# Kernel tuning notes

Hardware: AMD Instinct MI355X
Metric: run time of the kernel (lower is better)

## Reference

```python
import jax, jax.numpy as jnp
import numpy as np

HEADS = 8
HEAD_DIM = 64
WINDOW = 65  # odd


def setup_inputs() -> dict:
    key = jax.random.key(0)
    k1, k2, k3 = jax.random.split(key, 3)
    B, S, D_MODEL = 2, 2048, HEADS * HEAD_DIM
    x = jax.random.normal(k1, (B, S, D_MODEL), dtype=jnp.float32)
    W_qkv = jax.random.normal(k2, (D_MODEL, 3 * HEADS * HEAD_DIM), dtype=jnp.float32) * (1.0 / np.sqrt(D_MODEL))
    W_out = jax.random.normal(k3, (HEADS * HEAD_DIM, D_MODEL), dtype=jnp.float32) * (1.0 / np.sqrt(HEADS * HEAD_DIM))
    b_out = jnp.zeros((D_MODEL,), dtype=jnp.float32)
    return {"x": x, "W_qkv": W_qkv, "W_out": W_out, "b_out": b_out}


def reference(x, W_qkv, W_out, b_out):
    B, S, _ = x.shape
    H, D, W = HEADS, HEAD_DIM, WINDOW
    pad = W // 2

    qkv = x @ W_qkv                              # [B,S,3*H*D]
    qkv = qkv.reshape(B, S, H, 3 * D)
    q, k, v = jnp.split(qkv, 3, axis=-1)          # each [B,S,H,D]

    # zero-pad along sequence (matches tf.pad; padded keys get score 0, NOT -inf)
    k_pad = jnp.pad(k, ((0, 0), (pad, pad), (0, 0), (0, 0)))
    v_pad = jnp.pad(v, ((0, 0), (pad, pad), (0, 0), (0, 0)))

    # sliding windows via gather: [S, W] indices into padded seq (= tf.signal.frame)
    idx = jnp.arange(S)[:, None] + jnp.arange(W)[None, :]
    k_win = k_pad[:, idx]                         # [B,S,W,H,D]
    v_win = v_pad[:, idx]                         # [B,S,W,H,D]

    scale = 1.0 / jnp.sqrt(jnp.asarray(D, dtype=x.dtype))
    scores = jnp.einsum('bshd,bswhd->bhsw', q, k_win) * scale  # [B,H,S,W]
    weights = jax.nn.softmax(scores, axis=-1)
    attn = jnp.einsum('bhsw,bswhd->bshd', weights, v_win)       # [B,S,H,D]
    attn = attn.reshape(B, S, H * D)
    return attn @ W_out + b_out
```

## Files before the change

kernel.cpp:

```cpp
#include <hip/hip_runtime.h>
#include <hip/hip_bf16.h>
#include <stdint.h>

typedef short short8 __attribute__((ext_vector_type(8)));
typedef float f32x4 __attribute__((ext_vector_type(4)));
typedef unsigned short ushort4_t __attribute__((ext_vector_type(4)));
typedef unsigned short ushort8_t __attribute__((ext_vector_type(8)));

#define S_LEN 2048
#define NQKV 1536
#define DMODEL 512

__device__ inline unsigned short f2bf(float f) {
  unsigned int u = __float_as_uint(f);
  unsigned int r = (u + 0x7FFFu + ((u >> 16) & 1u)) >> 16;
  return (unsigned short)r;
}

__device__ __forceinline__ void gll16(const unsigned short* g, unsigned short* l) {
  __builtin_amdgcn_global_load_lds(
      (const __attribute__((address_space(1))) unsigned int*)g,
      (__attribute__((address_space(3))) unsigned int*)l, 16, 0, 0);
}

__global__ __launch_bounds__(256) void k_prep(const float* __restrict__ x,
                                              unsigned short* __restrict__ xb,
                                              const float* __restrict__ w1,
                                              unsigned short* __restrict__ o1,
                                              const float* __restrict__ w2,
                                              unsigned short* __restrict__ o2) {
  __shared__ float T[32][33];
  int bid = blockIdx.x;
  int t = threadIdx.x;
  if (bid < 1024) {
    int i = (bid * 256 + t) * 8;
    float4 a = *(const float4*)(x + i);
    float4 b = *(const float4*)(x + i + 4);
    ushort8_t o;
    o[0] = f2bf(a.x); o[1] = f2bf(a.y); o[2] = f2bf(a.z); o[3] = f2bf(a.w);
    o[4] = f2bf(b.x); o[5] = f2bf(b.y); o[6] = f2bf(b.z); o[7] = f2bf(b.w);
    *(ushort8_t*)(xb + i) = o;
    return;
  }
  bid -= 1024;
  int bx = bid & 63, byy = bid >> 6;
  const float* w; unsigned short* o; int cols;
  if (bx < 48) { w = w1; o = o1; cols = 1536; }
  else         { w = w2; o = o2; cols = 512; bx -= 48; }
  int r0 = byy * 32, c0 = bx * 32;
  int tr = t / 32, tc = t % 32;
#pragma unroll
  for (int i = 0; i < 4; i++) {
    int r = tr + i * 8;
    T[r][tc] = w[(size_t)(r0 + r) * cols + c0 + tc];
  }
  __syncthreads();
#pragma unroll
  for (int i = 0; i < 4; i++) {
    int rr = tr + i * 8;
    o[(size_t)(c0 + rr) * 512 + r0 + tc] = f2bf(T[tc][rr]);
  }
}

template <int BM, int MODE>
__global__ __launch_bounds__(256) void k_gemm(const unsigned short* __restrict__ A,
                                              const unsigned short* __restrict__ Bt,
                                              void* __restrict__ Cout,
                                              const float* __restrict__ bias,
                                              unsigned short* __restrict__ vt,
                                              int M, int N, int K) {
  constexpr int MR = BM / 32;
  constexpr int CA = BM / 64;
  constexpr int STAGE_SH = 2 * BM * 32 + 2 * 128 * 32;
  constexpr int SMEM_SH = (MODE == 1 && 128 * 128 > STAGE_SH) ? 128 * 128 : STAGE_SH;
  __shared__ __align__(16) unsigned short smem[SMEM_SH];
  const int ASZ = BM * 32, BOFF = 2 * BM * 32, BSZ = 128 * 32;

  const int t = threadIdx.x, lane = t & 63, wid = t >> 6;
  const int m0 = blockIdx.y * BM, n0 = blockIdx.x * 128;
  const int wm = (wid >> 1) * (BM / 2), wn = (wid & 1) * 64;
  const int lr = lane & 15, kr = (lane >> 4) * 8, lg = lane >> 4;
  const unsigned short* Ab = A + (size_t)m0 * K;
  const unsigned short* Bb = Bt + (size_t)n0 * K;
  f32x4 acc[MR][4] = {};

  const int NT = K / 32;
  auto stage = [&](int buf, int kt) {
#pragma unroll
    for (int c = 0; c < CA; c++) {
      int f = t + 256 * c;
      gll16(Ab + (size_t)(f >> 2) * K + kt + (f & 3) * 8, &smem[buf * ASZ + f * 8]);
    }
#pragma unroll
    for (int c = 0; c < 2; c++) {
      int f = t + 256 * c;
      gll16(Bb + (size_t)(f >> 2) * K + kt + (f & 3) * 8, &smem[BOFF + buf * BSZ + f * 8]);
    }
  };

  stage(0, 0);
  int buf = 0;
  for (int it = 0; it < NT; ++it) {
    __syncthreads();
    if (it + 1 < NT) stage(buf ^ 1, (it + 1) * 32);
    const unsigned short* Ap = &smem[buf * ASZ];
    const unsigned short* Bp = &smem[BOFF + buf * BSZ];
    short8 af[MR], bfv[4];
#pragma unroll
    for (int i = 0; i < MR; i++)
      af[i] = *(const short8*)&Ap[(wm + i * 16 + lr) * 32 + kr];
#pragma unroll
    for (int i = 0; i < 4; i++)
      bfv[i] = *(const short8*)&Bp[(wn + i * 16 + lr) * 32 + kr];
#pragma unroll
    for (int mi = 0; mi < MR; mi++)
#pragma unroll
      for (int ni = 0; ni < 4; ni++)
        acc[mi][ni] = __builtin_amdgcn_mfma_f32_16x16x32_bf16(af[mi], bfv[ni], acc[mi][ni], 0, 0, 0);
    buf ^= 1;
  }

  if (MODE == 0) {
#pragma unroll
    for (int mi = 0; mi < MR; mi++) {
#pragma unroll
      for (int ni = 0; ni < 4; ni++) {
        int col = n0 + wn + ni * 16 + lr;
        float bv = bias[col];
#pragma unroll
        for (int j = 0; j < 4; j++) {
          int row = m0 + wm + mi * 16 + lg * 4 + j;
          ((float*)Cout)[(size_t)row * N + col] = acc[mi][ni][j] + bv;
        }
      }
    }
  } else {
    __syncthreads();
#pragma unroll
    for (int mi = 0; mi < MR; mi++)
#pragma unroll
      for (int ni = 0; ni < 4; ni++)
#pragma unroll
        for (int j = 0; j < 4; j++) {
          int row = wm + mi * 16 + lg * 4 + j;
          int col = wn + ni * 16 + lr;
          smem[row * 128 + (col ^ (((row >> 3) & 7) << 3))] = f2bf(acc[mi][ni][j]);
        }
    __syncthreads();

    unsigned short* qkvout = (unsigned short*)Cout;
    const int b_ = m0 >> 11;
    const int posb = m0 & 2047;
#pragma unroll
    for (int hf = 0; hf < 2; hf++) {
      int c_abs = n0 + hf * 64;
      int g = c_abs % 192;
      if (g < 128) {
#pragma unroll
        for (int i = 0; i < 4; i++) {
          int s = t + 256 * i;
          int row = s >> 3, ch = s & 7;
          int src = row * 128 + ((hf * 64 + ch * 8) ^ (((row >> 3) & 7) << 3));
          ushort8_t v = *(const ushort8_t*)&smem[src];
          *(ushort8_t*)&qkvout[(size_t)(m0 + row) * NQKV + c_abs + ch * 8] = v;
        }
      } else {
        int h = c_abs / 192, d0 = g - 128;
#pragma unroll
        for (int i = 0; i < 4; i++) {
          int s = t + 256 * i;
          int dl = s >> 4, pc = s & 15;
          ushort8_t v;
#pragma unroll
          for (int j = 0; j < 8; j++) {
            int row = pc * 8 + j;
            v[j] = smem[row * 128 + ((hf * 64 + dl) ^ (((row >> 3) & 7) << 3))];
          }
          *(ushort8_t*)&vt[((size_t)((b_ * 8 + h) * 64 + d0 + dl)) * 2048 + posb + pc * 8] = v;
        }
      }
    }
  }
}

__global__ __launch_bounds__(256) void k_attn(const unsigned short* __restrict__ qkv,
                                              const unsigned short* __restrict__ vT,
                                              unsigned short* __restrict__ attn) {
  const int t = threadIdx.x, lane = t & 63, w = t >> 6;
  const int blk = blockIdx.x;
  const int sbi = blk & 31, h = (blk >> 5) & 7, b = blk >> 8;
  const int sb = sbi * 64;
  const unsigned short* base = qkv + (size_t)b * S_LEN * NQKV;
  const int lr = lane & 15, lg = lane >> 4;
  const int s0 = sb + w * 16;

  short8 qb[2];
#pragma unroll
  for (int ks = 0; ks < 2; ks++)
    qb[ks] = *(const short8*)(base + (size_t)(s0 + lr) * NQKV + h * 192 + ks * 32 + lg * 8);

  f32x4 sc[5] = {};
#pragma unroll
  for (int ct = 0; ct < 5; ct++) {
    int p = s0 - 32 + ct * 16 + lr;
    bool inb = (p >= 0 && p < S_LEN);
#pragma unroll
    for (int ks = 0; ks < 2; ks++) {
      short8 ka = {};
      if (inb)
        ka = *(const short8*)(base + (size_t)p * NQKV + h * 192 + 64 + ks * 32 + lg * 8);
      sc[ct] = __builtin_amdgcn_mfma_f32_16x16x32_bf16(ka, qb[ks], sc[ct], 0, 0, 0);
    }
  }

  float mx = -1e30f;
#pragma unroll
  for (int ct = 0; ct < 5; ct++)
#pragma unroll
    for (int j = 0; j < 4; j++) {
      int c2 = ct * 16 + lg * 4 + j;
      sc[ct][j] = (c2 >= lr && c2 <= lr + 64) ? sc[ct][j] * 0.125f : -1e30f;
      mx = fmaxf(mx, sc[ct][j]);
    }
  mx = fmaxf(mx, __shfl_xor(mx, 16, 64));
  mx = fmaxf(mx, __shfl_xor(mx, 32, 64));

  float pn[5][4];
  float sum = 0.0f;
#pragma unroll
  for (int ct = 0; ct < 5; ct++)
#pragma unroll
    for (int j = 0; j < 4; j++) {
      pn[ct][j] = __expf(sc[ct][j] - mx);
      sum += pn[ct][j];
    }
  sum += __shfl_xor(sum, 16, 64);
  sum += __shfl_xor(sum, 32, 64);
  float inv = 1.0f / sum;

  unsigned int w01[5], w23[5];
#pragma unroll
  for (int ct = 0; ct < 5; ct++) {
    float v[4];
#pragma unroll
    for (int j = 0; j < 4; j++) {
      int p = s0 - 32 + ct * 16 + lg * 4 + j;
      float xv = pn[ct][j] * inv;
      v[j] = (p >= 0 && p < S_LEN) ? xv : 0.0f;
    }
    w01[ct] = (unsigned int)f2bf(v[0]) | ((unsigned int)f2bf(v[1]) << 16);
    w23[ct] = (unsigned int)f2bf(v[2]) | ((unsigned int)f2bf(v[3]) << 16);
  }

  const unsigned short* vbase = vT + (size_t)((b * 8 + h) * 64) * 2048;
  f32x4 oa[4] = {};
  const int h2 = lg & 1, tl = lg >> 1;
  const int sA = 32 * h2 + lr, sB = sA + 16;
#pragma unroll
  for (int ks = 0; ks < 3; ks++) {
    const int T0 = 2 * ks;
    const int T1 = (2 * ks + 1 < 5) ? (2 * ks + 1) : 4;
    unsigned int a0 = __shfl((int)w01[T0], sA, 64), a1 = __shfl((int)w23[T0], sA, 64);
    unsigned int a2 = __shfl((int)w01[T0], sB, 64), a3 = __shfl((int)w23[T0], sB, 64);
    unsigned int b0 = __shfl((int)w01[T1], sA, 64), b1 = __shfl((int)w23[T1], sA, 64);
    unsigned int b2 = __shfl((int)w01[T1], sB, 64), b3 = __shfl((int)w23[T1], sB, 64);
    union { unsigned int u[4]; short8 v; } pb;
    pb.u[0] = tl ? b0 : a0;
    pb.u[1] = tl ? b1 : a1;
    pb.u[2] = tl ? b2 : a2;
    pb.u[3] = tl ? b3 : a3;
    if (ks == 2 && tl) { pb.u[0] = 0; pb.u[1] = 0; pb.u[2] = 0; pb.u[3] = 0; }
    int poff = s0 - 32 + ks * 32 + lg * 8;
#pragma unroll
    for (int nt = 0; nt < 4; nt++) {
      short8 va = *(const short8*)(vbase + (size_t)(nt * 16 + lr) * 2048 + poff);
      oa[nt] = __builtin_amdgcn_mfma_f32_16x16x32_bf16(va, pb.v, oa[nt], 0, 0, 0);
    }
  }

#pragma unroll
  for (int nt = 0; nt < 4; nt++) {
    ushort4_t o;
#pragma unroll
    for (int j = 0; j < 4; j++) o[j] = f2bf(oa[nt][j]);
    *(ushort4_t*)(attn + ((size_t)b * S_LEN + s0 + lr) * DMODEL + h * 64 + nt * 16 + lg * 4) = o;
  }
}

extern "C" void kernel_launch(void* const* d_in, const int* in_sizes, int n_in,
                              void* d_out, int out_size, void* d_ws, size_t ws_size,
                              hipStream_t stream) {
  const float* x    = (const float*)d_in[0];
  const float* Wqkv = (const float*)d_in[1];
  const float* Wout = (const float*)d_in[2];
  const float* bout = (const float*)d_in[3];
  char* ws = (char*)d_ws;
  unsigned short* xb    = (unsigned short*)(ws + 0);
  unsigned short* wqkvt = (unsigned short*)(ws + 4194304);
  unsigned short* woutt = (unsigned short*)(ws + 5767168);
  unsigned short* qkv   = (unsigned short*)(ws + 6291456);
  unsigned short* attn  = (unsigned short*)(ws + 18874368);
  unsigned short* vT    = (unsigned short*)(ws + 23068672);

  hipLaunchKernelGGL(k_prep, dim3(2048), dim3(256), 0, stream,
                     x, xb, Wqkv, wqkvt, Wout, woutt);
  hipLaunchKernelGGL((k_gemm<128, 1>), dim3(12, 32), dim3(256), 0, stream,
                     xb, wqkvt, (void*)qkv, (const float*)nullptr, vT, 4096, 1536, 512);
  hipLaunchKernelGGL(k_attn, dim3(512), dim3(256), 0, stream, qkv, vT, attn);
  hipLaunchKernelGGL((k_gemm<64, 0>), dim3(4, 64), dim3(256), 0, stream,
                     attn, woutt, d_out, bout, (unsigned short*)nullptr, 4096, 512, 512);
}
```

Baseline: 44.31 us.

## Store Q/K/V in per-head zero-padded layouts and stage attention tiles in LDS

The QKV GEMM epilogue now writes Q as contiguous per-head rows, and writes K and V (transposed) into per-head buffers padded by 32 zero rows on each side. The padding is cleared by extra blocks in the prep kernel. The attention kernel loads its K, V and Q tiles into swizzled LDS with async global-to-LDS loads instead of strided global reads, which removes the per-element bounds checks and masking. The output GEMM epilogue now goes through LDS so it can write coalesced float4 stores with the bias added. The cost is more LDS use in the attention kernel and extra zero-fill work in the prep kernel.

```diff
diff --git a/kernel.cpp b/kernel.cpp
--- a/kernel.cpp
+++ b/kernel.cpp
@@ -28,7 +28,9 @@
                                               const float* __restrict__ w1,
                                               unsigned short* __restrict__ o1,
                                               const float* __restrict__ w2,
-                                              unsigned short* __restrict__ o2) {
+                                              unsigned short* __restrict__ o2,
+                                              unsigned short* __restrict__ Kp,
+                                              unsigned short* __restrict__ Vp) {
   __shared__ float T[32][33];
   int bid = blockIdx.x;
   int t = threadIdx.x;
@@ -42,6 +44,29 @@
     *(ushort8_t*)(xb + i) = o;
     return;
   }
+  if (bid >= 2048) {
+    int p = bid - 2048;
+    ushort8_t z = {};
+    if (p < 16) {
+      unsigned short* dst = Kp + (size_t)p * 2112 * 64;
+#pragma unroll
+      for (int i = 0; i < 2; i++) {
+        int s = t + 256 * i;
+        int row = s >> 3, c = s & 7;
+        int r2 = row < 32 ? row : row - 32 + 2080;
+        *(ushort8_t*)&dst[r2 * 64 + c * 8] = z;
+      }
+    } else {
+      unsigned short* dst = Vp + (size_t)(p - 16) * 64 * 2112;
+#pragma unroll
+      for (int i = 0; i < 2; i++) {
+        int s = t + 256 * i;
+        int d = s >> 3, side = (s >> 2) & 1, c = s & 3;
+        *(ushort8_t*)&dst[(size_t)d * 2112 + side * 2080 + c * 8] = z;
+      }
+    }
+    return;
+  }
   bid -= 1024;
   int bx = bid & 63, byy = bid >> 6;
   const float* w; unsigned short* o; int cols;
@@ -67,12 +92,15 @@
                                               const unsigned short* __restrict__ Bt,
                                               void* __restrict__ Cout,
                                               const float* __restrict__ bias,
-                                              unsigned short* __restrict__ vt,
+                                              unsigned short* __restrict__ qs,
+                                              unsigned short* __restrict__ kp,
+                                              unsigned short* __restrict__ vp,
                                               int M, int N, int K) {
   constexpr int MR = BM / 32;
   constexpr int CA = BM / 64;
   constexpr int STAGE_SH = 2 * BM * 32 + 2 * 128 * 32;
-  constexpr int SMEM_SH = (MODE == 1 && 128 * 128 > STAGE_SH) ? 128 * 128 : STAGE_SH;
+  constexpr int BOUNCE_SH = 16384;
+  constexpr int SMEM_SH = STAGE_SH > BOUNCE_SH ? STAGE_SH : BOUNCE_SH;
   __shared__ __align__(16) unsigned short smem[SMEM_SH];
   const int ASZ = BM * 32, BOFF = 2 * BM * 32, BSZ = 128 * 32;
 
@@ -121,18 +149,24 @@
   }
 
   if (MODE == 0) {
-#pragma unroll
-    for (int mi = 0; mi < MR; mi++) {
-#pragma unroll
-      for (int ni = 0; ni < 4; ni++) {
-        int col = n0 + wn + ni * 16 + lr;
-        float bv = bias[col];
-#pragma unroll
-        for (int j = 0; j < 4; j++) {
-          int row = m0 + wm + mi * 16 + lg * 4 + j;
-          ((float*)Cout)[(size_t)row * N + col] = acc[mi][ni][j] + bv;
-        }
-      }
+    __syncthreads();
+    float* ft = (float*)smem;
+#pragma unroll
+    for (int mi = 0; mi < MR; mi++)
+#pragma unroll
+      for (int ni = 0; ni < 4; ni++)
+#pragma unroll
+        for (int j = 0; j < 4; j++)
+          ft[(wm + mi * 16 + lg * 4 + j) * 128 + wn + ni * 16 + lr] = acc[mi][ni][j];
+    __syncthreads();
+#pragma unroll
+    for (int i = 0; i < BM / 8; i++) {
+      int s = t + 256 * i;
+      int row = s >> 5, ch = s & 31;
+      float4 v = *(const float4*)&ft[row * 128 + ch * 4];
+      float4 bv = *(const float4*)&bias[n0 + ch * 4];
+      v.x += bv.x; v.y += bv.y; v.z += bv.z; v.w += bv.w;
+      *(float4*)&((float*)Cout)[(size_t)(m0 + row) * N + n0 + ch * 4] = v;
     }
   } else {
     __syncthreads();
@@ -148,24 +182,25 @@
         }
     __syncthreads();
 
-    unsigned short* qkvout = (unsigned short*)Cout;
     const int b_ = m0 >> 11;
     const int posb = m0 & 2047;
 #pragma unroll
     for (int hf = 0; hf < 2; hf++) {
       int c_abs = n0 + hf * 64;
-      int g = c_abs % 192;
-      if (g < 128) {
+      int h = c_abs / 192, seg = (c_abs % 192) >> 6;
+      if (seg < 2) {
+        unsigned short* dst = (seg == 0)
+            ? qs + ((size_t)(b_ * 8 + h) * 2048 + posb) * 64
+            : kp + ((size_t)(b_ * 8 + h) * 2112 + 32 + posb) * 64;
 #pragma unroll
         for (int i = 0; i < 4; i++) {
           int s = t + 256 * i;
           int row = s >> 3, ch = s & 7;
           int src = row * 128 + ((hf * 64 + ch * 8) ^ (((row >> 3) & 7) << 3));
-          ushort8_t v = *(const ushort8_t*)&smem[src];
-          *(ushort8_t*)&qkvout[(size_t)(m0 + row) * NQKV + c_abs + ch * 8] = v;
+          *(ushort8_t*)&dst[s * 8] = *(const ushort8_t*)&smem[src];
         }
       } else {
-        int h = c_abs / 192, d0 = g - 128;
+        unsigned short* dst = vp + (size_t)(b_ * 8 + h) * 64 * 2112;
 #pragma unroll
         for (int i = 0; i < 4; i++) {
           int s = t + 256 * i;
@@ -176,39 +211,66 @@
             int row = pc * 8 + j;
             v[j] = smem[row * 128 + ((hf * 64 + dl) ^ (((row >> 3) & 7) << 3))];
           }
-          *(ushort8_t*)&vt[((size_t)((b_ * 8 + h) * 64 + d0 + dl)) * 2048 + posb + pc * 8] = v;
+          *(ushort8_t*)&dst[(size_t)dl * 2112 + 32 + posb + pc * 8] = v;
         }
       }
     }
   }
 }
 
-__global__ __launch_bounds__(256) void k_attn(const unsigned short* __restrict__ qkv,
-                                              const unsigned short* __restrict__ vT,
-                                              unsigned short* __restrict__ attn) {
+__global__ __launch_bounds__(256) void k_attn(const unsigned short* __restrict__ Qs,
+                                              const unsigned short* __restrict__ Kp,
+                                              const unsigned short* __restrict__ Vp,
+                                              unsigned short* __restrict__ attnb) {
+  __shared__ __align__(16) unsigned short Kt[128 * 64];
+  __shared__ __align__(16) unsigned short Vt[64 * 192];
+  __shared__ __align__(16) unsigned short Qt[64 * 64];
   const int t = threadIdx.x, lane = t & 63, w = t >> 6;
   const int blk = blockIdx.x;
   const int sbi = blk & 31, h = (blk >> 5) & 7, b = blk >> 8;
   const int sb = sbi * 64;
-  const unsigned short* base = qkv + (size_t)b * S_LEN * NQKV;
+  const int bh = b * 8 + h;
   const int lr = lane & 15, lg = lane >> 4;
-  const int s0 = sb + w * 16;
+
+  {
+    const unsigned short* src = Kp + ((size_t)bh * 2112 + sb) * 64;
+#pragma unroll
+    for (int i = 0; i < 4; i++) {
+      int s = t + 256 * i, row = s >> 3, c = s & 7;
+      gll16(src + row * 64 + (c ^ (row & 7)) * 8, &Kt[s * 8]);
+    }
+  }
+  {
+    const unsigned short* src = Vp + (size_t)bh * 64 * 2112 + sb;
+#pragma unroll
+    for (int i = 0; i < 6; i++) {
+      int s = t + 256 * i, d = s / 24, c = s - d * 24;
+      gll16(src + (size_t)d * 2112 + (c ^ (d & 7)) * 8, &Vt[s * 8]);
+    }
+  }
+  {
+    const unsigned short* src = Qs + ((size_t)bh * 2048 + sb) * 64;
+#pragma unroll
+    for (int i = 0; i < 2; i++) {
+      int s = t + 256 * i, row = s >> 3, c = s & 7;
+      gll16(src + row * 64 + (c ^ (row & 7)) * 8, &Qt[s * 8]);
+    }
+  }
+  __syncthreads();
+
+  const int sw = (lr & 7) << 3;
 
   short8 qb[2];
 #pragma unroll
   for (int ks = 0; ks < 2; ks++)
-    qb[ks] = *(const short8*)(base + (size_t)(s0 + lr) * NQKV + h * 192 + ks * 32 + lg * 8);
+    qb[ks] = *(const short8*)&Qt[(w * 16 + lr) * 64 + ((ks * 32 + lg * 8) ^ sw)];
 
   f32x4 sc[5] = {};
 #pragma unroll
   for (int ct = 0; ct < 5; ct++) {
-    int p = s0 - 32 + ct * 16 + lr;
-    bool inb = (p >= 0 && p < S_LEN);
 #pragma unroll
     for (int ks = 0; ks < 2; ks++) {
-      short8 ka = {};
-      if (inb)
-        ka = *(const short8*)(base + (size_t)p * NQKV + h * 192 + 64 + ks * 32 + lg * 8);
+      short8 ka = *(const short8*)&Kt[(w * 16 + ct * 16 + lr) * 64 + ((ks * 32 + lg * 8) ^ sw)];
       sc[ct] = __builtin_amdgcn_mfma_f32_16x16x32_bf16(ka, qb[ks], sc[ct], 0, 0, 0);
     }
   }
@@ -241,18 +303,10 @@
   unsigned int w01[5], w23[5];
 #pragma unroll
   for (int ct = 0; ct < 5; ct++) {
-    float v[4];
-#pragma unroll
-    for (int j = 0; j < 4; j++) {
-      int p = s0 - 32 + ct * 16 + lg * 4 + j;
-      float xv = pn[ct][j] * inv;
-      v[j] = (p >= 0 && p < S_LEN) ? xv : 0.0f;
-    }
-    w01[ct] = (unsigned int)f2bf(v[0]) | ((unsigned int)f2bf(v[1]) << 16);
-    w23[ct] = (unsigned int)f2bf(v[2]) | ((unsigned int)f2bf(v[3]) << 16);
-  }
-
-  const unsigned short* vbase = vT + (size_t)((b * 8 + h) * 64) * 2048;
+    w01[ct] = (unsigned int)f2bf(pn[ct][0] * inv) | ((unsigned int)f2bf(pn[ct][1] * inv) << 16);
+    w23[ct] = (unsigned int)f2bf(pn[ct][2] * inv) | ((unsigned int)f2bf(pn[ct][3] * inv) << 16);
+  }
+
   f32x4 oa[4] = {};
   const int h2 = lg & 1, tl = lg >> 1;
   const int sA = 32 * h2 + lr, sB = sA + 16;
@@ -270,20 +324,21 @@
     pb.u[2] = tl ? b2 : a2;
     pb.u[3] = tl ? b3 : a3;
     if (ks == 2 && tl) { pb.u[0] = 0; pb.u[1] = 0; pb.u[2] = 0; pb.u[3] = 0; }
-    int poff = s0 - 32 + ks * 32 + lg * 8;
+    int pofl = w * 16 + ks * 32 + lg * 8;
 #pragma unroll
     for (int nt = 0; nt < 4; nt++) {
-      short8 va = *(const short8*)(vbase + (size_t)(nt * 16 + lr) * 2048 + poff);
+      short8 va = *(const short8*)&Vt[(nt * 16 + lr) * 192 + (pofl ^ sw)];
       oa[nt] = __builtin_amdgcn_mfma_f32_16x16x32_bf16(va, pb.v, oa[nt], 0, 0, 0);
     }
   }
 
+  const int s0 = sb + w * 16;
 #pragma unroll
   for (int nt = 0; nt < 4; nt++) {
     ushort4_t o;
 #pragma unroll
     for (int j = 0; j < 4; j++) o[j] = f2bf(oa[nt][j]);
-    *(ushort4_t*)(attn + ((size_t)b * S_LEN + s0 + lr) * DMODEL + h * 64 + nt * 16 + lg * 4) = o;
+    *(ushort4_t*)&attnb[((size_t)b * S_LEN + s0 + lr) * DMODEL + h * 64 + nt * 16 + lg * 4] = o;
   }
 }
 
@@ -298,15 +353,18 @@
   unsigned short* xb    = (unsigned short*)(ws + 0);
   unsigned short* wqkvt = (unsigned short*)(ws + 4194304);
   unsigned short* woutt = (unsigned short*)(ws + 5767168);
-  unsigned short* qkv   = (unsigned short*)(ws + 6291456);
-  unsigned short* attn  = (unsigned short*)(ws + 18874368);
-  unsigned short* vT    = (unsigned short*)(ws + 23068672);
-
-  hipLaunchKernelGGL(k_prep, dim3(2048), dim3(256), 0, stream,
-                     x, xb, Wqkv, wqkvt, Wout, woutt);
+  unsigned short* Qs    = (unsigned short*)(ws + 6291456);
+  unsigned short* Kp    = (unsigned short*)(ws + 10485760);
+  unsigned short* Vp    = (unsigned short*)(ws + 14811136);
+  unsigned short* attnb = (unsigned short*)(ws + 19922944);
+
+  hipLaunchKernelGGL(k_prep, dim3(2080), dim3(256), 0, stream,
+                     x, xb, Wqkv, wqkvt, Wout, woutt, Kp, Vp);
   hipLaunchKernelGGL((k_gemm<128, 1>), dim3(12, 32), dim3(256), 0, stream,
-                     xb, wqkvt, (void*)qkv, (const float*)nullptr, vT, 4096, 1536, 512);
-  hipLaunchKernelGGL(k_attn, dim3(512), dim3(256), 0, stream, qkv, vT, attn);
+                     xb, wqkvt, nullptr, (const float*)nullptr, Qs, Kp, Vp, 4096, 1536, 512);
+  hipLaunchKernelGGL(k_attn, dim3(512), dim3(256), 0, stream, Qs, Kp, Vp, attnb);
   hipLaunchKernelGGL((k_gemm<64, 0>), dim3(4, 64), dim3(256), 0, stream,
-                     attn, woutt, d_out, bout, (unsigned short*)nullptr, 4096, 512, 512);
-}
+                     attnb, woutt, d_out, bout,
+                     (unsigned short*)nullptr, (unsigned short*)nullptr,
+                     (unsigned short*)nullptr, 4096, 512, 512);
+}
```

Measured after the change: 42.34 us. 1.05x faster.
